# Optimization experiments

Measured on AMD Instinct MI355X. Metric: run time of the kernel, lower is better.

Reference implementation:

```python
import jax, jax.numpy as jnp
import numpy as np

INPUT_DIM, HIDDEN_DIM, OUTPUT_DIM, NUM_LAYERS = 128, 512, 128, 2
B, T = 32, 2048


def setup_inputs() -> dict:
    key = jax.random.key(0)
    ks = jax.random.split(key, 11)
    s_in = 1.0 / np.sqrt(HIDDEN_DIM)
    inp = {"x": jax.random.normal(ks[0], (B, T, INPUT_DIM), dtype=jnp.float32)}
    # layer 0 (input_dim -> hidden), layer 1 (hidden -> hidden); PyTorch gate order i,f,g,o
    inp["w_ih0"] = jax.random.uniform(ks[1], (4 * HIDDEN_DIM, INPUT_DIM), minval=-s_in, maxval=s_in)
    inp["w_hh0"] = jax.random.uniform(ks[2], (4 * HIDDEN_DIM, HIDDEN_DIM), minval=-s_in, maxval=s_in)
    inp["b_ih0"] = jax.random.uniform(ks[3], (4 * HIDDEN_DIM,), minval=-s_in, maxval=s_in)
    inp["b_hh0"] = jax.random.uniform(ks[4], (4 * HIDDEN_DIM,), minval=-s_in, maxval=s_in)
    inp["w_ih1"] = jax.random.uniform(ks[5], (4 * HIDDEN_DIM, HIDDEN_DIM), minval=-s_in, maxval=s_in)
    inp["w_hh1"] = jax.random.uniform(ks[6], (4 * HIDDEN_DIM, HIDDEN_DIM), minval=-s_in, maxval=s_in)
    inp["b_ih1"] = jax.random.uniform(ks[7], (4 * HIDDEN_DIM,), minval=-s_in, maxval=s_in)
    inp["b_hh1"] = jax.random.uniform(ks[8], (4 * HIDDEN_DIM,), minval=-s_in, maxval=s_in)
    inp["fc_w"] = jax.random.uniform(ks[9], (OUTPUT_DIM, HIDDEN_DIM), minval=-s_in, maxval=s_in)
    inp["fc_b"] = jax.random.uniform(ks[10], (OUTPUT_DIM,), minval=-s_in, maxval=s_in)
    return inp


def _lstm_layer(x, w_ih, w_hh, b_ih, b_hh):
    # x: [B, T, D] -> hidden states [B, T, H], final (h, c) each [B, H]
    b, t, _ = x.shape
    h4 = w_hh.shape[0]
    H = h4 // 4
    # precompute input projections for all timesteps (one big GEMM)
    x_proj = jnp.einsum('btd,gd->btg', x, w_ih) + b_ih + b_hh  # [B, T, 4H]

    def step(carry, xt):
        h, c = carry
        gates = xt + h @ w_hh.T  # [B, 4H]
        i, f, g, o = jnp.split(gates, 4, axis=-1)
        i = jax.nn.sigmoid(i)
        f = jax.nn.sigmoid(f)
        g = jnp.tanh(g)
        o = jax.nn.sigmoid(o)
        c = f * c + i * g
        h = o * jnp.tanh(c)
        return (h, c), h

    init = (jnp.zeros((b, H), x.dtype), jnp.zeros((b, H), x.dtype))
    (h_n, c_n), hs = jax.lax.scan(step, init, jnp.swapaxes(x_proj, 0, 1))
    return jnp.swapaxes(hs, 0, 1), h_n, c_n


def reference(x, w_ih0, w_hh0, b_ih0, b_hh0, w_ih1, w_hh1, b_ih1, b_hh1, fc_w, fc_b):
    out0, h0, c0 = _lstm_layer(x, w_ih0, w_hh0, b_ih0, b_hh0)
    out1, h1, c1 = _lstm_layer(out0, w_ih1, w_hh1, b_ih1, b_hh1)
    h_n = jnp.stack([h0, h1])  # [L, B, H]
    c_n = jnp.stack([c0, c1])  # [L, B, H]
    # fc(relu(.)) applied once over all (batch, time) -- collapses the Python loop
    output = jnp.einsum('bth,oh->bto', jax.nn.relu(out1), fc_w) + fc_b  # [B, T, O]
    hidden = jnp.einsum('lbh,oh->lbo', jax.nn.relu(h_n), fc_w) + fc_b   # [L, B, O]
    return jnp.squeeze(output), hidden, c_n
```

## Files before the change

kernel.cpp:

```cpp
#include <hip/hip_runtime.h>

typedef unsigned int u32;
typedef unsigned short u16;
typedef unsigned long long u64;

#define T_STEPS 2048
#define BATCH   32
#define HID     512
#define INDIM   128
#define OUTD    128
#define NG      2048
#define L0_WGS  64
#define L1_WGS  64
#define FC_WGS  4
#define NWG     (L0_WGS + L1_WGS + FC_WGS)
#define BH      (BATCH * HID)

#define HID_OFF 8388608
#define CN_OFF  8396800

#define WS_FLAGS   0
#define WS_H0RING  16384
#define WS_H1RING  (WS_H0RING + 131072)
#define WS_BIAS0   (WS_H1RING + 131072)
#define WS_BIAS1   (WS_BIAS0 + 8192)
#define WS_WFC     (WS_BIAS1 + 8192)
#define WS_WL0     (WS_WFC + 131072)
#define WS_WL1     (WS_WL0 + 2621440)
#define WS_XBF     (WS_WL1 + 4194304)
#define WS_H0DEEP  (WS_XBF + 16777216)
#define WS_H1DEEP  (WS_H0DEEP + 67141632)
#define WS_DEEPEND (WS_H1DEEP + 67141632)

typedef __bf16 bf16x8 __attribute__((ext_vector_type(8)));
typedef float  f32x4  __attribute__((ext_vector_type(4)));
typedef unsigned int u32x4 __attribute__((ext_vector_type(4)));

__device__ __forceinline__ u16 f2bf(float f) {
    u32 u = __float_as_uint(f);
    u32 r = u + 0x7FFFu + ((u >> 16) & 1u);
    return (u16)(r >> 16);
}

union UB2 { u32x4 u; bf16x8 b; };
__device__ __forceinline__ bf16x8 as_bf(u32x4 u) { UB2 x; x.u = u; return x.b; }

__device__ __forceinline__ u32 relu2(u32 u) {
    u32 lo = (u & 0x8000u)     ? 0u : (u & 0xFFFFu);
    u32 hi = (u & 0x80000000u) ? 0u : (u & 0xFFFF0000u);
    return lo | hi;
}

__device__ __forceinline__ u32x4 ld16_llc(const void* p) {
    u32x4 r;
    asm volatile("global_load_dwordx4 %0, %1, off sc0 sc1"
                 : "=v"(r) : "v"(p) : "memory");
    return r;
}
__device__ __forceinline__ u32x4 ld16_l2(const void* p) {
    u32x4 r;
    asm volatile("global_load_dwordx4 %0, %1, off sc0"
                 : "=v"(r) : "v"(p) : "memory");
    return r;
}
__device__ __forceinline__ void wait_vm0() {
    asm volatile("s_waitcnt vmcnt(0)" ::: "memory");
    __builtin_amdgcn_sched_barrier(0);
}
__device__ __forceinline__ void vm0() {
    asm volatile("s_waitcnt vmcnt(0)" ::: "memory");
}


__global__ void k_zero(u32* dst, int n) {
    int i = blockIdx.x * blockDim.x + threadIdx.x;
    if (i < n) dst[i] = 0u;
}

__global__ void k_bias(const float* __restrict__ bih0, const float* __restrict__ bhh0,
                       const float* __restrict__ bih1, const float* __restrict__ bhh1,
                       float* __restrict__ bias0, float* __restrict__ bias1) {
    int i = blockIdx.x * blockDim.x + threadIdx.x;
    if (i < NG) {
        int orig = (i & 3) * HID + (i >> 2);
        bias0[i] = bih0[orig] + bhh0[orig];
        bias1[i] = bih1[orig] + bhh1[orig];
    }
}

__global__ void k_xconv(const float* __restrict__ x, u16* __restrict__ xbf) {
    int i = blockIdx.x * blockDim.x + threadIdx.x;
    float4 v = reinterpret_cast<const float4*>(x)[i];
    u32 lo = (u32)f2bf(v.x) | ((u32)f2bf(v.y) << 16);
    u32 hi = (u32)f2bf(v.z) | ((u32)f2bf(v.w) << 16);
    reinterpret_cast<uint2*>(xbf)[i] = make_uint2(lo, hi);
}

__global__ void k_wconv(const float* __restrict__ wih0, const float* __restrict__ whh0,
                        const float* __restrict__ wih1, const float* __restrict__ whh1,
                        const float* __restrict__ fcw,
                        u16* __restrict__ wl0, u16* __restrict__ wl1, u16* __restrict__ wfc) {
    int i = blockIdx.x * blockDim.x + threadIdx.x;
    if (i < 64 * 20480) {
        int wg = i / 20480, r = i % 20480;
        int ks = r / 1024, kb = (r % 1024) / 256, n = (r % 256) / 8, j = r % 8;
        int k = ks * 32 + kb * 8 + j;
        int p = wg * 32 + n;
        int orig = (p & 3) * HID + (p >> 2);
        float v = (k < HID) ? whh0[orig * HID + k] : wih0[orig * INDIM + (k - HID)];
        wl0[i] = f2bf(v);
        return;
    }
    int i1 = i - 64 * 20480;
    if (i1 < 64 * 32768) {
        int wg = i1 / 32768, r = i1 % 32768;
        int ks = r / 1024, kb = (r % 1024) / 256, n = (r % 256) / 8, j = r % 8;
        int k = ks * 32 + kb * 8 + j;
        int p = wg * 32 + n;
        int orig = (p & 3) * HID + (p >> 2);
        float v = (k < HID) ? wih1[orig * HID + k] : whh1[orig * HID + (k - HID)];
        wl1[i1] = f2bf(v);
        return;
    }
    int i2 = i1 - 64 * 32768;
    if (i2 < 4 * 16384) {
        int wg = i2 / 16384, r = i2 % 16384;
        int ks = r / 1024, kb = (r % 1024) / 256, n = (r % 256) / 8, j = r % 8;
        int k = ks * 32 + kb * 8 + j;
        int o = wg * 32 + n;
        wfc[i2] = f2bf(fcw[o * HID + k]);
    }
}


__global__ __launch_bounds__(256, 1)
void k_lstm(const u16* __restrict__ xbf,
            const u16* __restrict__ wl0g, const u16* __restrict__ wl1g, const u16* __restrict__ wfcg,
            const float* __restrict__ bias0, const float* __restrict__ bias1, const float* __restrict__ fcb,
            u16* __restrict__ h0ring, u16* __restrict__ h1ring,
            u32* __restrict__ flags, float* __restrict__ dout, const int deep)
{
    __shared__ u16   wlds[32768];
    __shared__ u32x4 hstage[2][2048];
    const int tid  = threadIdx.x;
    const int lane = tid & 63;
    const int wv   = tid >> 6;
    const int mt   = wv >> 1;
    const int nt   = wv & 1;
    const int ci   = lane & 15;
    const int quad = lane >> 4;
    const int wg   = blockIdx.x;

    int role, rwg;
    if      (wg < L0_WGS)           { role = 0; rwg = wg; }
    else if (wg < L0_WGS + L1_WGS)  { role = 1; rwg = wg - L0_WGS; }
    else                            { role = 2; rwg = wg - L0_WGS - L1_WGS; }

    u32* flagL0 = flags;
    u32* flagL1 = flags + 64 * 16;
    u32* flagFC = flags + 128 * 16;
    u32* myflag = flags + wg * 16;

    {
        const u16* src = (role == 0) ? (wl0g + rwg * 20480)
                       : (role == 1) ? (wl1g + rwg * 32768)
                                     : (wfcg + rwg * 16384);
        const int n4 = (role == 0) ? 2560 : (role == 1) ? 4096 : 2048;
        uint4* d4 = reinterpret_cast<uint4*>(wlds);
        const uint4* s4 = reinterpret_cast<const uint4*>(src);
        for (int i = tid; i < n4; i += 256) d4[i] = s4[i];
    }
    __syncthreads();

    const bf16x8* wp = reinterpret_cast<const bf16x8*>(wlds);
    const int wbase  = quad * 32 + nt * 16 + ci;
    const int pcol   = rwg * 32 + nt * 16 + ci;
    const int gateid = pcol & 3;
    const float bias = (role == 0) ? bias0[pcol] : (role == 1) ? bias1[pcol] : fcb[pcol];
    const int brow0  = mt * 16 + quad * 4;
    const int arow   = mt * 16 + ci;
    const int jidx   = pcol >> 2;
    const int hfrag  = arow * 64 + quad;
    const int hswz   = arow & 7;

    float cst[4] = {0.f, 0.f, 0.f, 0.f};

    auto spin = [&](u32* f, int target) {
        if (target > 0)
            while ((int)__hip_atomic_load(f, __ATOMIC_RELAXED, __HIP_MEMORY_SCOPE_AGENT) < target)
                __builtin_amdgcn_s_sleep(1);
    };

    auto rdIdx = [&](int t_h) -> long {
        return deep ? (long)(t_h + 1) : (long)(t_h & 3);
    };

    auto stage1 = [&](const u16* slot, int buf) {
        u32x4 b[8];
        if (deep) {
            #pragma unroll
            for (int r = 0; r < 8; ++r) b[r] = ld16_l2(slot + (tid + r * 256) * 8);
        } else {
            #pragma unroll
            for (int r = 0; r < 8; ++r) b[r] = ld16_llc(slot + (tid + r * 256) * 8);
        }
        wait_vm0();
        #pragma unroll
        for (int r = 0; r < 8; ++r) {
            int c = tid + r * 256;
            hstage[buf][c ^ ((c >> 6) & 7)] = b[r];
        }
    };
    auto stage2 = [&](const u16* s0, const u16* s1) {
        u32x4 b0[8], b1[8];
        if (deep) {
            #pragma unroll
            for (int r = 0; r < 8; ++r) b0[r] = ld16_l2(s0 + (tid + r * 256) * 8);
            #pragma unroll
            for (int r = 0; r < 8; ++r) b1[r] = ld16_l2(s1 + (tid + r * 256) * 8);
        } else {
            #pragma unroll
            for (int r = 0; r < 8; ++r) b0[r] = ld16_llc(s0 + (tid + r * 256) * 8);
            #pragma unroll
            for (int r = 0; r < 8; ++r) b1[r] = ld16_llc(s1 + (tid + r * 256) * 8);
        }
        wait_vm0();
        #pragma unroll
        for (int r = 0; r < 8; ++r) {
            int c = tid + r * 256;
            int cs = c ^ ((c >> 6) & 7);
            hstage[0][cs] = b0[r];
            hstage[1][cs] = b1[r];
        }
    };

    auto epi = [&](const f32x4& acc, u16* slotb) {
        float ga[4], hv[4];
        #pragma unroll
        for (int r = 0; r < 4; ++r) {
            float g  = acc[r] + bias;
            float sv = 1.0f / (1.0f + __expf(-g));
            float tv = 1.0f - 2.0f / (__expf(2.0f * g) + 1.0f);
            ga[r] = (gateid == 2) ? tv : sv;
        }
        const int bl = lane & ~3;
        #pragma unroll
        for (int r = 0; r < 4; ++r) {
            float iv = __shfl(ga[r], bl + 0);
            float fv = __shfl(ga[r], bl + 1);
            float gv = __shfl(ga[r], bl + 2);
            float ov = __shfl(ga[r], bl + 3);
            float cn = fv * cst[r] + iv * gv;
            cst[r] = cn;
            hv[r] = ov * (1.0f - 2.0f / (__expf(2.0f * cn) + 1.0f));
        }
        u32 lo = 0, hi = 0;
        #pragma unroll
        for (int r = 0; r < 4; ++r) {
            float c0 = __shfl(hv[r], (quad << 4) + 0);
            float c1 = __shfl(hv[r], (quad << 4) + 4);
            float c2 = __shfl(hv[r], (quad << 4) + 8);
            float c3 = __shfl(hv[r], (quad << 4) + 12);
            if (ci == r) {
                lo = (u32)f2bf(c0) | ((u32)f2bf(c1) << 16);
                hi = (u32)f2bf(c2) | ((u32)f2bf(c3) << 16);
            }
        }
        if (ci < 4) {
            u64* dst = reinterpret_cast<u64*>(slotb) + (brow0 + ci) * 128 + rwg * 2 + nt;
            u64 val = (u64)lo | ((u64)hi << 32);
            __hip_atomic_store(dst, val, __ATOMIC_RELAXED, __HIP_MEMORY_SCOPE_AGENT);
        }
    };

    #define HMFMA16S(BUF, KSOFF)                                                 \
        _Pragma("unroll")                                                        \
        for (int _k = 0; _k < 16; ++_k) {                                        \
          u32x4 _hv = hstage[BUF][(hfrag + _k * 4) ^ hswz];                      \
          bf16x8 _bv = wp[wbase + (_k + (KSOFF)) * 128];                         \
          if (_k & 1) accB = __builtin_amdgcn_mfma_f32_16x16x32_bf16(as_bf(_hv), _bv, accB, 0, 0, 0); \
          else        accA = __builtin_amdgcn_mfma_f32_16x16x32_bf16(as_bf(_hv), _bv, accA, 0, 0, 0); \
        }

    auto fcTileS = [&](int buf) -> f32x4 {
        f32x4 accA = {0.f,0.f,0.f,0.f}, accB = {0.f,0.f,0.f,0.f};
        #pragma unroll
        for (int ks = 0; ks < 16; ++ks) {
            u32x4 v = hstage[buf][(hfrag + ks * 4) ^ hswz];
            v[0] = relu2(v[0]); v[1] = relu2(v[1]); v[2] = relu2(v[2]); v[3] = relu2(v[3]);
            bf16x8 bv = wp[wbase + ks * 128];
            if (ks & 1) accB = __builtin_amdgcn_mfma_f32_16x16x32_bf16(as_bf(v), bv, accB, 0, 0, 0);
            else        accA = __builtin_amdgcn_mfma_f32_16x16x32_bf16(as_bf(v), bv, accA, 0, 0, 0);
        }
        return accA + accB;
    };

    if (role == 0) {
        u32* pf = (tid < 64) ? (flagL0 + tid * 16)
                : (!deep && tid < 128) ? (flagL1 + (tid - 64) * 16) : nullptr;
        const int po = (tid < 64) ? 0 : -3;
        for (int t = 0; t < T_STEPS; ++t) {
            const u16* xA = xbf + (arow * T_STEPS + t) * INDIM + quad * 8;
            f32x4 accA = {0.f, 0.f, 0.f, 0.f}, accB = {0.f, 0.f, 0.f, 0.f};
            u32x4 xv[4];
            #pragma unroll
            for (int k4 = 0; k4 < 4; ++k4) xv[k4] = *reinterpret_cast<const u32x4*>(xA + k4 * 32);
            #pragma unroll
            for (int k4 = 0; k4 < 4; ++k4) {
                bf16x8 bv = wp[wbase + (16 + k4) * 128];
                if (k4 & 1) accB = __builtin_amdgcn_mfma_f32_16x16x32_bf16(as_bf(xv[k4]), bv, accB, 0, 0, 0);
                else        accA = __builtin_amdgcn_mfma_f32_16x16x32_bf16(as_bf(xv[k4]), bv, accA, 0, 0, 0);
            }
            if (pf) spin(pf, t + po);
            __syncthreads();
            stage1(h0ring + rdIdx(t - 1) * BH, 0);
            __syncthreads();
            HMFMA16S(0, 0);
            epi(accA + accB, h0ring + rdIdx(t) * BH);
            vm0();
            __syncthreads();
            if (tid == 0)
                __hip_atomic_store(myflag, (u32)(t + 1), __ATOMIC_RELAXED, __HIP_MEMORY_SCOPE_AGENT);
        }
    } else if (role == 1) {
        u32* pf = (tid < 64)  ? (flagL0 + tid * 16)
                : (tid < 128) ? (flagL1 + (tid - 64) * 16)
                : (!deep && tid < 132) ? (flagFC + (tid - 128) * 16) : nullptr;
        const int po = (tid < 64) ? 1 : (tid < 128) ? 0 : -3;
        for (int t = 0; t < T_STEPS; ++t) {
            if (pf) spin(pf, t + po);
            __syncthreads();
            stage2(h0ring + rdIdx(t) * BH,
                   h1ring + rdIdx(t - 1) * BH);
            __syncthreads();
            f32x4 accA = {0.f, 0.f, 0.f, 0.f}, accB = {0.f, 0.f, 0.f, 0.f};
            HMFMA16S(0, 0);
            HMFMA16S(1, 16);
            epi(accA + accB, h1ring + rdIdx(t) * BH);
            vm0();
            __syncthreads();
            if (tid == 0)
                __hip_atomic_store(myflag, (u32)(t + 1), __ATOMIC_RELAXED, __HIP_MEMORY_SCOPE_AGENT);
        }
    } else {
        u32* pf = (tid < 64) ? (flagL1 + tid * 16) : nullptr;
        for (int t = 0; t < T_STEPS; ++t) {
            if (pf) spin(pf, t + 1);
            __syncthreads();
            stage1(h1ring + rdIdx(t) * BH, 0);
            __syncthreads();
            f32x4 acc = fcTileS(0);
            #pragma unroll
            for (int r = 0; r < 4; ++r)
                dout[((brow0 + r) * T_STEPS + t) * OUTD + pcol] = acc[r] + bias;
            __syncthreads();
            if (tid == 0)
                __hip_atomic_store(myflag, (u32)(t + 1), __ATOMIC_RELAXED, __HIP_MEMORY_SCOPE_AGENT);
        }
        stage1(h0ring + rdIdx(T_STEPS - 1) * BH, 1);
        __syncthreads();
        f32x4 hh1 = fcTileS(0);
        f32x4 hh0 = fcTileS(1);
        #pragma unroll
        for (int r = 0; r < 4; ++r)
            dout[HID_OFF + (brow0 + r) * OUTD + pcol] = hh0[r] + bias;
        #pragma unroll
        for (int r = 0; r < 4; ++r)
            dout[HID_OFF + (BATCH + brow0 + r) * OUTD + pcol] = hh1[r] + bias;
    }

    if (role <= 1 && (ci & 3) == 0) {
        #pragma unroll
        for (int r = 0; r < 4; ++r)
            dout[CN_OFF + (role * BATCH + brow0 + r) * HID + jidx] = cst[r];
    }
}


extern "C" void kernel_launch(void* const* d_in, const int* in_sizes, int n_in,
                              void* d_out, int out_size, void* d_ws, size_t ws_size,
                              hipStream_t stream) {
    const float* x    = (const float*)d_in[0];
    const float* wih0 = (const float*)d_in[1];
    const float* whh0 = (const float*)d_in[2];
    const float* bih0 = (const float*)d_in[3];
    const float* bhh0 = (const float*)d_in[4];
    const float* wih1 = (const float*)d_in[5];
    const float* whh1 = (const float*)d_in[6];
    const float* bih1 = (const float*)d_in[7];
    const float* bhh1 = (const float*)d_in[8];
    const float* fcw  = (const float*)d_in[9];
    const float* fcb  = (const float*)d_in[10];

    char* ws = (char*)d_ws;
    u32*  flags = (u32*)(ws + WS_FLAGS);
    float* b0   = (float*)(ws + WS_BIAS0);
    float* b1   = (float*)(ws + WS_BIAS1);
    u16*  wfc   = (u16*)(ws + WS_WFC);
    u16*  wl0   = (u16*)(ws + WS_WL0);
    u16*  wl1   = (u16*)(ws + WS_WL1);
    u16*  xbf   = (u16*)(ws + WS_XBF);
    float* dout = (float*)d_out;

    const int deep = (ws_size >= (size_t)WS_DEEPEND) ? 1 : 0;
    u16* h0r = deep ? (u16*)(ws + WS_H0DEEP) : (u16*)(ws + WS_H0RING);
    u16* h1r = deep ? (u16*)(ws + WS_H1DEEP) : (u16*)(ws + WS_H1RING);

    if (deep) {
        k_zero<<<16, 256, 0, stream>>>((u32*)ws, 4096);
        k_zero<<<32, 256, 0, stream>>>((u32*)(ws + WS_H0DEEP), 8192);
        k_zero<<<32, 256, 0, stream>>>((u32*)(ws + WS_H1DEEP), 8192);
    } else {
        k_zero<<<272, 256, 0, stream>>>((u32*)ws, 69632);
    }
    k_bias<<<8, 256, 0, stream>>>(bih0, bhh0, bih1, bhh1, b0, b1);
    k_xconv<<<8192, 256, 0, stream>>>(x, xbf);
    k_wconv<<<13568, 256, 0, stream>>>(wih0, whh0, wih1, whh1, fcw, wl0, wl1, wfc);
    k_lstm<<<NWG, 256, 0, stream>>>(xbf, wl0, wl1, wfc, b0, b1, fcb,
                                    h0r, h1r, flags, dout, deep);
}
```

Baseline: 9.059 ms.

## Replace per-step flag spinning with NaN-poisoned data-ready polling in deep ring

In the deep-buffer path, the per-timestep flag handshake between workgroups is removed. Consumers instead poll the hidden-state slots themselves, retrying any 16-byte chunk that still holds a NaN poison pattern. The host pre-fills the whole deep history buffers with poison each call, which drops the flag store, flag spin, and extra barrier from every step. In exchange it adds two large fill kernels per launch, and it would misbehave if a real bf16 hidden value ever matched the poison bits.

```diff
diff --git a/kernel.cpp b/kernel.cpp
--- a/kernel.cpp
+++ b/kernel.cpp
@@ -15,6 +15,8 @@
 #define FC_WGS  4
 #define NWG     (L0_WGS + L1_WGS + FC_WGS)
 #define BH      (BATCH * HID)
+#define SLOT_Q  4096
+#define POISON  0x7FC07FC0u
 
 #define HID_OFF 8388608
 #define CN_OFF  8396800
@@ -57,12 +59,6 @@
                  : "=v"(r) : "v"(p) : "memory");
     return r;
 }
-__device__ __forceinline__ u32x4 ld16_l2(const void* p) {
-    u32x4 r;
-    asm volatile("global_load_dwordx4 %0, %1, off sc0"
-                 : "=v"(r) : "v"(p) : "memory");
-    return r;
-}
 __device__ __forceinline__ void wait_vm0() {
     asm volatile("s_waitcnt vmcnt(0)" ::: "memory");
     __builtin_amdgcn_sched_barrier(0);
@@ -75,6 +71,11 @@
 __global__ void k_zero(u32* dst, int n) {
     int i = blockIdx.x * blockDim.x + threadIdx.x;
     if (i < n) dst[i] = 0u;
+}
+
+__global__ void k_fill(uint4* dst, int n16, u32 v) {
+    int i = blockIdx.x * blockDim.x + threadIdx.x;
+    if (i < n16) dst[i] = make_uint4(v, v, v, v);
 }
 
 __global__ void k_bias(const float* __restrict__ bih0, const float* __restrict__ bhh0,
@@ -190,51 +191,57 @@
             while ((int)__hip_atomic_load(f, __ATOMIC_RELAXED, __HIP_MEMORY_SCOPE_AGENT) < target)
                 __builtin_amdgcn_s_sleep(1);
     };
-
-    auto rdIdx = [&](int t_h) -> long {
-        return deep ? (long)(t_h + 1) : (long)(t_h & 3);
-    };
-
-    auto stage1 = [&](const u16* slot, int buf) {
-        u32x4 b[8];
-        if (deep) {
-            #pragma unroll
-            for (int r = 0; r < 8; ++r) b[r] = ld16_l2(slot + (tid + r * 256) * 8);
-        } else {
-            #pragma unroll
-            for (int r = 0; r < 8; ++r) b[r] = ld16_llc(slot + (tid + r * 256) * 8);
-        }
-        wait_vm0();
+    auto stf = [&](u32* f, u32 v) {
+        __hip_atomic_store(f, v, __ATOMIC_RELAXED, __HIP_MEMORY_SCOPE_AGENT);
+    };
+
+    auto slotQ = [&](u16* ring, int t_h) -> u64* {
+        long idx = deep ? (long)(t_h + 1) : (long)(t_h & 3);
+        return reinterpret_cast<u64*>(ring) + idx * SLOT_Q;
+    };
+
+    auto scat = [&](int buf, u32x4* b) {
         #pragma unroll
         for (int r = 0; r < 8; ++r) {
             int c = tid + r * 256;
             hstage[buf][c ^ ((c >> 6) & 7)] = b[r];
         }
     };
-    auto stage2 = [&](const u16* s0, const u16* s1) {
+
+    auto retry8 = [&](const u64* sq, u32x4* b) {
+        u32 need = 0xFFu;
+        while (__any((int)need)) {
+            #pragma unroll
+            for (int r = 0; r < 8; ++r)
+                if (need & (1u << r)) b[r] = ld16_llc(sq + 2 * (tid + r * 256));
+            wait_vm0();
+            #pragma unroll
+            for (int r = 0; r < 8; ++r)
+                if ((need & (1u << r)) && b[r][0] != POISON && b[r][2] != POISON)
+                    need &= ~(1u << r);
+            if (__any((int)need)) __builtin_amdgcn_s_sleep(1);
+        }
+    };
+
+    auto stage1f = [&](const u64* sq, int buf) {
+        u32x4 b[8];
+        #pragma unroll
+        for (int r = 0; r < 8; ++r) b[r] = ld16_llc(sq + 2 * (tid + r * 256));
+        wait_vm0();
+        scat(buf, b);
+    };
+    auto stage2f = [&](const u64* s0, const u64* s1) {
         u32x4 b0[8], b1[8];
-        if (deep) {
-            #pragma unroll
-            for (int r = 0; r < 8; ++r) b0[r] = ld16_l2(s0 + (tid + r * 256) * 8);
-            #pragma unroll
-            for (int r = 0; r < 8; ++r) b1[r] = ld16_l2(s1 + (tid + r * 256) * 8);
-        } else {
-            #pragma unroll
-            for (int r = 0; r < 8; ++r) b0[r] = ld16_llc(s0 + (tid + r * 256) * 8);
-            #pragma unroll
-            for (int r = 0; r < 8; ++r) b1[r] = ld16_llc(s1 + (tid + r * 256) * 8);
-        }
+        #pragma unroll
+        for (int r = 0; r < 8; ++r) b0[r] = ld16_llc(s0 + 2 * (tid + r * 256));
+        #pragma unroll
+        for (int r = 0; r < 8; ++r) b1[r] = ld16_llc(s1 + 2 * (tid + r * 256));
         wait_vm0();
-        #pragma unroll
-        for (int r = 0; r < 8; ++r) {
-            int c = tid + r * 256;
-            int cs = c ^ ((c >> 6) & 7);
-            hstage[0][cs] = b0[r];
-            hstage[1][cs] = b1[r];
-        }
-    };
-
-    auto epi = [&](const f32x4& acc, u16* slotb) {
+        scat(0, b0);
+        scat(1, b1);
+    };
+
+    auto epi = [&](const f32x4& acc, u64* sq) {
         float ga[4], hv[4];
         #pragma unroll
         for (int r = 0; r < 4; ++r) {
@@ -267,7 +274,7 @@
             }
         }
         if (ci < 4) {
-            u64* dst = reinterpret_cast<u64*>(slotb) + (brow0 + ci) * 128 + rwg * 2 + nt;
+            u64* dst = sq + (brow0 + ci) * 128 + rwg * 2 + nt;
             u64 val = (u64)lo | ((u64)hi << 32);
             __hip_atomic_store(dst, val, __ATOMIC_RELAXED, __HIP_MEMORY_SCOPE_AGENT);
         }
@@ -295,84 +302,160 @@
         return accA + accB;
     };
 
+    auto xpart = [&](int t, f32x4& aA, f32x4& aB) {
+        const u16* xA = xbf + (arow * T_STEPS + t) * INDIM + quad * 8;
+        u32x4 xv[4];
+        #pragma unroll
+        for (int k4 = 0; k4 < 4; ++k4) xv[k4] = *reinterpret_cast<const u32x4*>(xA + k4 * 32);
+        #pragma unroll
+        for (int k4 = 0; k4 < 4; ++k4) {
+            bf16x8 bv = wp[wbase + (16 + k4) * 128];
+            if (k4 & 1) aB = __builtin_amdgcn_mfma_f32_16x16x32_bf16(as_bf(xv[k4]), bv, aB, 0, 0, 0);
+            else        aA = __builtin_amdgcn_mfma_f32_16x16x32_bf16(as_bf(xv[k4]), bv, aA, 0, 0, 0);
+        }
+    };
+
     if (role == 0) {
-        u32* pf = (tid < 64) ? (flagL0 + tid * 16)
-                : (!deep && tid < 128) ? (flagL1 + (tid - 64) * 16) : nullptr;
-        const int po = (tid < 64) ? 0 : -3;
-        for (int t = 0; t < T_STEPS; ++t) {
-            const u16* xA = xbf + (arow * T_STEPS + t) * INDIM + quad * 8;
-            f32x4 accA = {0.f, 0.f, 0.f, 0.f}, accB = {0.f, 0.f, 0.f, 0.f};
-            u32x4 xv[4];
-            #pragma unroll
-            for (int k4 = 0; k4 < 4; ++k4) xv[k4] = *reinterpret_cast<const u32x4*>(xA + k4 * 32);
-            #pragma unroll
-            for (int k4 = 0; k4 < 4; ++k4) {
-                bf16x8 bv = wp[wbase + (16 + k4) * 128];
-                if (k4 & 1) accB = __builtin_amdgcn_mfma_f32_16x16x32_bf16(as_bf(xv[k4]), bv, accB, 0, 0, 0);
-                else        accA = __builtin_amdgcn_mfma_f32_16x16x32_bf16(as_bf(xv[k4]), bv, accA, 0, 0, 0);
-            }
-            if (pf) spin(pf, t + po);
+        if (deep) {
+            for (int t = 0; t < T_STEPS; ++t) {
+                f32x4 accA = {0.f,0.f,0.f,0.f}, accB = {0.f,0.f,0.f,0.f};
+                xpart(t, accA, accB);
+                u32x4 b[8];
+                retry8(slotQ(h0ring, t - 1), b);
+                __syncthreads();
+                scat(0, b);
+                __syncthreads();
+                HMFMA16S(0, 0);
+                epi(accA + accB, slotQ(h0ring, t));
+            }
+        } else {
+            u32* pf = (tid < 64) ? (flagL0 + tid * 16) : (tid < 128) ? (flagL1 + (tid - 64) * 16) : nullptr;
+            const int po = (tid < 64) ? 0 : -3;
+            for (int t = 0; t < T_STEPS; ++t) {
+                f32x4 accA = {0.f,0.f,0.f,0.f}, accB = {0.f,0.f,0.f,0.f};
+                xpart(t, accA, accB);
+                if (pf) spin(pf, t + po);
+                __syncthreads();
+                stage1f(slotQ(h0ring, t - 1), 0);
+                __syncthreads();
+                HMFMA16S(0, 0);
+                epi(accA + accB, slotQ(h0ring, t));
+                vm0();
+                __syncthreads();
+                if (tid == 0) stf(myflag, (u32)(t + 1));
+            }
+        }
+        if ((ci & 3) == 0) {
+            #pragma unroll
+            for (int r = 0; r < 4; ++r)
+                dout[CN_OFF + (brow0 + r) * HID + jidx] = cst[r];
+        }
+    } else if (role == 1) {
+        if (deep) {
+            for (int t = 0; t < T_STEPS; ++t) {
+                u32x4 b0[8], b1[8];
+                u32 n0 = 0xFFu, n1 = 0xFFu;
+                const u64* s0 = slotQ(h0ring, t);
+                const u64* s1 = slotQ(h1ring, t - 1);
+                while (__any((int)(n0 | n1))) {
+                    #pragma unroll
+                    for (int r = 0; r < 8; ++r)
+                        if (n1 & (1u << r)) b1[r] = ld16_llc(s1 + 2 * (tid + r * 256));
+                    #pragma unroll
+                    for (int r = 0; r < 8; ++r)
+                        if (n0 & (1u << r)) b0[r] = ld16_llc(s0 + 2 * (tid + r * 256));
+                    wait_vm0();
+                    #pragma unroll
+                    for (int r = 0; r < 8; ++r) {
+                        if ((n1 & (1u << r)) && b1[r][0] != POISON && b1[r][2] != POISON) n1 &= ~(1u << r);
+                        if ((n0 & (1u << r)) && b0[r][0] != POISON && b0[r][2] != POISON) n0 &= ~(1u << r);
+                    }
+                    if (__any((int)(n0 | n1))) __builtin_amdgcn_s_sleep(1);
+                }
+                __syncthreads();
+                scat(0, b0);
+                scat(1, b1);
+                __syncthreads();
+                f32x4 accA = {0.f,0.f,0.f,0.f}, accB = {0.f,0.f,0.f,0.f};
+                HMFMA16S(0, 0);
+                HMFMA16S(1, 16);
+                epi(accA + accB, slotQ(h1ring, t));
+            }
+        } else {
+            u32* pf = (tid < 64)  ? (flagL0 + tid * 16)
+                    : (tid < 128) ? (flagL1 + (tid - 64) * 16)
+                    : (tid < 132) ? (flagFC + (tid - 128) * 16) : nullptr;
+            const int po = (tid < 64) ? 1 : (tid < 128) ? 0 : -3;
+            for (int t = 0; t < T_STEPS; ++t) {
+                if (pf) spin(pf, t + po);
+                __syncthreads();
+                stage2f(slotQ(h0ring, t), slotQ(h1ring, t - 1));
+                __syncthreads();
+                f32x4 accA = {0.f,0.f,0.f,0.f}, accB = {0.f,0.f,0.f,0.f};
+                HMFMA16S(0, 0);
+                HMFMA16S(1, 16);
+                epi(accA + accB, slotQ(h1ring, t));
+                vm0();
+                __syncthreads();
+                if (tid == 0) stf(myflag, (u32)(t + 1));
+            }
+        }
+        if ((ci & 3) == 0) {
+            #pragma unroll
+            for (int r = 0; r < 4; ++r)
+                dout[CN_OFF + (BATCH + brow0 + r) * HID + jidx] = cst[r];
+        }
+    } else {
+        if (deep) {
+            for (int t = 0; t < T_STEPS; ++t) {
+                u32x4 b[8];
+                retry8(slotQ(h1ring, t), b);
+                __syncthreads();
+                scat(0, b);
+                __syncthreads();
+                f32x4 acc = fcTileS(0);
+                #pragma unroll
+                for (int r = 0; r < 4; ++r)
+                    dout[((brow0 + r) * T_STEPS + t) * OUTD + pcol] = acc[r] + bias;
+            }
+            f32x4 hh1 = fcTileS(0);
+            u32x4 b[8];
+            retry8(slotQ(h0ring, T_STEPS - 1), b);
             __syncthreads();
-            stage1(h0ring + rdIdx(t - 1) * BH, 0);
+            scat(1, b);
             __syncthreads();
-            HMFMA16S(0, 0);
-            epi(accA + accB, h0ring + rdIdx(t) * BH);
-            vm0();
+            f32x4 hh0 = fcTileS(1);
+            #pragma unroll
+            for (int r = 0; r < 4; ++r)
+                dout[HID_OFF + (brow0 + r) * OUTD + pcol] = hh0[r] + bias;
+            #pragma unroll
+            for (int r = 0; r < 4; ++r)
+                dout[HID_OFF + (BATCH + brow0 + r) * OUTD + pcol] = hh1[r] + bias;
+        } else {
+            u32* pf = (tid < 64) ? (flagL1 + tid * 16) : nullptr;
+            for (int t = 0; t < T_STEPS; ++t) {
+                if (pf) spin(pf, t + 1);
+                __syncthreads();
+                stage1f(slotQ(h1ring, t), 0);
+                __syncthreads();
+                f32x4 acc = fcTileS(0);
+                #pragma unroll
+                for (int r = 0; r < 4; ++r)
+                    dout[((brow0 + r) * T_STEPS + t) * OUTD + pcol] = acc[r] + bias;
+                __syncthreads();
+                if (tid == 0) stf(myflag, (u32)(t + 1));
+            }
+            stage1f(slotQ(h0ring, T_STEPS - 1), 1);
             __syncthreads();
-            if (tid == 0)
-                __hip_atomic_store(myflag, (u32)(t + 1), __ATOMIC_RELAXED, __HIP_MEMORY_SCOPE_AGENT);
-        }
-    } else if (role == 1) {
-        u32* pf = (tid < 64)  ? (flagL0 + tid * 16)
-                : (tid < 128) ? (flagL1 + (tid - 64) * 16)
-                : (!deep && tid < 132) ? (flagFC + (tid - 128) * 16) : nullptr;
-        const int po = (tid < 64) ? 1 : (tid < 128) ? 0 : -3;
-        for (int t = 0; t < T_STEPS; ++t) {
-            if (pf) spin(pf, t + po);
-            __syncthreads();
-            stage2(h0ring + rdIdx(t) * BH,
-                   h1ring + rdIdx(t - 1) * BH);
-            __syncthreads();
-            f32x4 accA = {0.f, 0.f, 0.f, 0.f}, accB = {0.f, 0.f, 0.f, 0.f};
-            HMFMA16S(0, 0);
-            HMFMA16S(1, 16);
-            epi(accA + accB, h1ring + rdIdx(t) * BH);
-            vm0();
-            __syncthreads();
-            if (tid == 0)
-                __hip_atomic_store(myflag, (u32)(t + 1), __ATOMIC_RELAXED, __HIP_MEMORY_SCOPE_AGENT);
-        }
-    } else {
-        u32* pf = (tid < 64) ? (flagL1 + tid * 16) : nullptr;
-        for (int t = 0; t < T_STEPS; ++t) {
-            if (pf) spin(pf, t + 1);
-            __syncthreads();
-            stage1(h1ring + rdIdx(t) * BH, 0);
-            __syncthreads();
-            f32x4 acc = fcTileS(0);
+            f32x4 hh1 = fcTileS(0);
+            f32x4 hh0 = fcTileS(1);
             #pragma unroll
             for (int r = 0; r < 4; ++r)
-                dout[((brow0 + r) * T_STEPS + t) * OUTD + pcol] = acc[r] + bias;
-            __syncthreads();
-            if (tid == 0)
-                __hip_atomic_store(myflag, (u32)(t + 1), __ATOMIC_RELAXED, __HIP_MEMORY_SCOPE_AGENT);
-        }
-        stage1(h0ring + rdIdx(T_STEPS - 1) * BH, 1);
-        __syncthreads();
-        f32x4 hh1 = fcTileS(0);
-        f32x4 hh0 = fcTileS(1);
-        #pragma unroll
-        for (int r = 0; r < 4; ++r)
-            dout[HID_OFF + (brow0 + r) * OUTD + pcol] = hh0[r] + bias;
-        #pragma unroll
-        for (int r = 0; r < 4; ++r)
-            dout[HID_OFF + (BATCH + brow0 + r) * OUTD + pcol] = hh1[r] + bias;
-    }
-
-    if (role <= 1 && (ci & 3) == 0) {
-        #pragma unroll
-        for (int r = 0; r < 4; ++r)
-            dout[CN_OFF + (role * BATCH + brow0 + r) * HID + jidx] = cst[r];
+                dout[HID_OFF + (brow0 + r) * OUTD + pcol] = hh0[r] + bias;
+            #pragma unroll
+            for (int r = 0; r < 4; ++r)
+                dout[HID_OFF + (BATCH + brow0 + r) * OUTD + pcol] = hh1[r] + bias;
+        }
     }
 }
 
@@ -407,9 +490,10 @@
     u16* h1r = deep ? (u16*)(ws + WS_H1DEEP) : (u16*)(ws + WS_H1RING);
 
     if (deep) {
-        k_zero<<<16, 256, 0, stream>>>((u32*)ws, 4096);
         k_zero<<<32, 256, 0, stream>>>((u32*)(ws + WS_H0DEEP), 8192);
         k_zero<<<32, 256, 0, stream>>>((u32*)(ws + WS_H1DEEP), 8192);
+        k_fill<<<16384, 256, 0, stream>>>((uint4*)(ws + WS_H0DEEP + 32768), 4194304, POISON);
+        k_fill<<<16384, 256, 0, stream>>>((uint4*)(ws + WS_H1DEEP + 32768), 4194304, POISON);
     } else {
         k_zero<<<272, 256, 0, stream>>>((u32*)ws, 69632);
     }
```

Result: slower. 12.51 ms (+38.1%).
